# Performance work log

Measured on AMD Instinct MI355X. Metric: run time of the kernel, lower is better.

## Reference

```python
import jax, jax.numpy as jnp
import numpy as np

INF = 1e38  # matches torch source constant


def setup_inputs() -> dict:
    key = jax.random.key(0)
    k1, k2, k3 = jax.random.split(key, 3)
    B, N, D = 16, 2048, 512
    query = jax.random.normal(k1, (B, N, D), dtype=jnp.float32)
    # nn.Linear(dims, dims, bias=False): weight [out, in] = [D, D]
    W_in = jax.random.normal(k2, (D, D), dtype=jnp.float32) * (1.0 / np.sqrt(D))
    # nn.Linear(2*dims, dims, bias=False): weight [D, 2D]
    W_out = jax.random.normal(k3, (D, 2 * D), dtype=jnp.float32) * (1.0 / np.sqrt(2 * D))
    return {"query": query, "W_in": W_in, "W_out": W_out}


def reference(query, W_in, W_out):
    B, N, D = query.shape
    # linear_in: y = x @ W^T
    q = jnp.einsum("bnd,ed->bne", query, W_in)  # [B, N, D]
    # full QK^T scores
    scores = jnp.einsum("bnd,bmd->bnm", q, q)  # [B, N, N]
    # torch: scores[:, triu_mask] = -INF  -> mask upper triangle INCLUDING diagonal
    mask = jnp.triu(jnp.ones((N, N), dtype=bool))
    scores = jnp.where(mask, -INF, scores)
    weights = jax.nn.softmax(scores, axis=-1)
    # row 0 is all -INF -> softmax gives uniform; torch zeroes it explicitly
    weights = weights.at[:, 0, :].set(0.0)
    mix = jnp.einsum("bnm,bmd->bnd", weights, q)  # [B, N, D]
    combined = jnp.concatenate([mix, q], axis=-1)  # [B, N, 2D]
    # linear_out (no activation since activation=None)
    output = jnp.einsum("bnc,dc->bnd", combined, W_out)  # [B, N, D]
    return output
```

## Files before the change

kernel.cpp:

```cpp
#include <hip/hip_runtime.h>

typedef _Float16 f16;
typedef _Float16 half8 __attribute__((ext_vector_type(8)));
typedef _Float16 half4 __attribute__((ext_vector_type(4)));
typedef float floatx4 __attribute__((ext_vector_type(4)));
typedef unsigned int uintx4 __attribute__((ext_vector_type(4)));

#define MFMA16(a, b, c) __builtin_amdgcn_mfma_f32_16x16x32_f16(a, b, c, 0, 0, 0)

__device__ __forceinline__ void gload16(const void* g, void* l) {
    __builtin_amdgcn_global_load_lds((const __attribute__((address_space(1))) void*)g,
                                     (__attribute__((address_space(3))) void*)l, 16, 0, 0);
}

__global__ __launch_bounds__(256) void k_cvt(const float* __restrict__ query,
                                             const float* __restrict__ Wi,
                                             const float* __restrict__ Wo,
                                             f16* __restrict__ q16,
                                             f16* __restrict__ W16)
{
    int i = blockIdx.x * 256 + threadIdx.x;
    const float4* src;
    f16* dst;
    if (i < 4194304) { src = (const float4*)query + i; dst = q16 + (size_t)i * 4; }
    else if (i < 4259840) { int j = i - 4194304; src = (const float4*)Wi + j; dst = W16 + (size_t)j * 4; }
    else { int j = i - 4259840; src = (const float4*)Wo + j; dst = W16 + 262144 + (size_t)j * 4; }
    float4 v = *src;
    half4 h = {(f16)v.x, (f16)v.y, (f16)v.z, (f16)v.w};
    *reinterpret_cast<half4*>(dst) = h;
}

__global__ __launch_bounds__(256) void k_qin(const f16* __restrict__ q16,
                                             const f16* __restrict__ W16,
                                             f16* __restrict__ comb,
                                             f16* __restrict__ qT)
{
    __shared__ char sm[65536];
    const int tid = threadIdx.x, lane = tid & 63, w = tid >> 6;
    const int l15 = lane & 15, quad = lane >> 4;
    const int id = blockIdx.x, xcd = id & 7, u = id >> 3;
    const int mbase = (xcd * 32 + (u >> 2)) * 128;
    const int nbase = (u & 3) * 128;
    const int wm = (w & 1) * 64, wn = (w >> 1) * 64;
    const int ia = wm >> 4, jb = wn >> 4;

    floatx4 acc[4][4];
#pragma unroll
    for (int i = 0; i < 4; ++i)
#pragma unroll
        for (int j = 0; j < 4; ++j) acc[i][j] = (floatx4)0.f;

    auto STAGE = [&](int k0, int bsel) {
        f16* At = (f16*)(sm + bsel * 32768);
        f16* Bt = At + 8192;
#pragma unroll
        for (int jr = 0; jr < 4; ++jr) {
            int bi = jr * 4 + w, i2 = bi >> 1, s = bi & 1;
            gload16(q16 + (size_t)(mbase + i2 * 16 + l15) * 512 + k0 + s * 32 + quad * 8, At + bi * 512);
            gload16(W16 + (size_t)(nbase + i2 * 16 + l15) * 512 + k0 + s * 32 + quad * 8, Bt + bi * 512);
        }
    };

    STAGE(0, 0);
    __syncthreads();
    for (int it = 0; it < 8; ++it) {
        const int cur = it & 1;
        if (it < 7) STAGE((it + 1) * 64, cur ^ 1);
        f16* At = (f16*)(sm + cur * 32768);
        f16* Bt = At + 8192;
#pragma unroll
        for (int s = 0; s < 2; ++s) {
            half8 a[4], bf[4];
#pragma unroll
            for (int i = 0; i < 4; ++i)
                a[i] = *reinterpret_cast<half8*>(At + ((ia + i) * 2 + s) * 512 + lane * 8);
#pragma unroll
            for (int j = 0; j < 4; ++j)
                bf[j] = *reinterpret_cast<half8*>(Bt + ((jb + j) * 2 + s) * 512 + lane * 8);
#pragma unroll
            for (int i = 0; i < 4; ++i)
#pragma unroll
                for (int j = 0; j < 4; ++j)
                    acc[i][j] = MFMA16(a[i], bf[j], acc[i][j]);
        }
        __syncthreads();
    }
    const int bb = mbase >> 11, tb = mbase & 2047;
    f16* ct = (f16*)sm;
#pragma unroll
    for (int i = 0; i < 4; ++i)
#pragma unroll
        for (int j = 0; j < 4; ++j)
#pragma unroll
            for (int r = 0; r < 4; ++r)
                ct[(wm + i * 16 + quad * 4 + r) * 136 + wn + j * 16 + l15] = (f16)acc[i][j][r];
    __syncthreads();
#pragma unroll
    for (int it = 0; it < 8; ++it) {
        int c = it * 256 + tid, r = c >> 4, c8 = (c & 15) << 3;
        *reinterpret_cast<half8*>(comb + (size_t)(mbase + r) * 1024 + 512 + nbase + c8) =
            *reinterpret_cast<half8*>(ct + r * 136 + c8);
    }
    __syncthreads();
#pragma unroll
    for (int i = 0; i < 4; ++i)
#pragma unroll
        for (int j = 0; j < 4; ++j) {
            half4 h = {(f16)acc[i][j][0], (f16)acc[i][j][1], (f16)acc[i][j][2], (f16)acc[i][j][3]};
            *reinterpret_cast<half4*>(ct + (wn + j * 16 + l15) * 136 + wm + i * 16 + quad * 4) = h;
        }
    __syncthreads();
#pragma unroll
    for (int it = 0; it < 8; ++it) {
        int c = it * 256 + tid, dd = c >> 4, tc = (c & 15) << 3;
        *reinterpret_cast<half8*>(qT + ((size_t)bb * 512 + nbase + dd) * 2048 + tb + tc) =
            *reinterpret_cast<half8*>(ct + dd * 136 + tc);
    }
}

__global__ __launch_bounds__(256) void k_sgemmsm(const f16* __restrict__ comb,
                                                 f16* __restrict__ Pd,
                                                 float* __restrict__ Mt,
                                                 float* __restrict__ Lt)
{
    __shared__ char sm[65536];
    const int tid = threadIdx.x, lane = tid & 63, w = tid >> 6;
    const int l15 = lane & 15, quad = lane >> 4;
    const int wm = (w & 1) * 64, wn = (w >> 1) * 64;
    const int ia = wm >> 4, jb = wn >> 4;

    int bx = blockIdx.y, mt = 0;
    while ((mt + 1) * (mt + 2) / 2 <= bx) ++mt;
    const int nt = bx - mt * (mt + 1) / 2;
    const int b = blockIdx.x;
    const f16* qa = comb + ((size_t)b * 2048 + mt * 128) * 1024 + 512;
    const f16* qb = comb + ((size_t)b * 2048 + nt * 128) * 1024 + 512;

    floatx4 acc[4][4];
#pragma unroll
    for (int i = 0; i < 4; ++i)
#pragma unroll
        for (int j = 0; j < 4; ++j) acc[i][j] = (floatx4)0.f;

    auto STAGE = [&](int k0, int bsel) {
        f16* At = (f16*)(sm + bsel * 32768);
        f16* Bt = At + 8192;
#pragma unroll
        for (int jr = 0; jr < 4; ++jr) {
            int bi = jr * 4 + w, i2 = bi >> 1, s = bi & 1;
            gload16(qa + (size_t)(i2 * 16 + l15) * 1024 + k0 + s * 32 + quad * 8, At + bi * 512);
            gload16(qb + (size_t)(i2 * 16 + l15) * 1024 + k0 + s * 32 + quad * 8, Bt + bi * 512);
        }
    };

    STAGE(0, 0);
    __syncthreads();
    for (int it = 0; it < 8; ++it) {
        const int cur = it & 1;
        if (it < 7) STAGE((it + 1) * 64, cur ^ 1);
        f16* At = (f16*)(sm + cur * 32768);
        f16* Bt = At + 8192;
#pragma unroll
        for (int s = 0; s < 2; ++s) {
            half8 a[4], bf[4];
#pragma unroll
            for (int i = 0; i < 4; ++i)
                a[i] = *reinterpret_cast<half8*>(At + ((ia + i) * 2 + s) * 512 + lane * 8);
#pragma unroll
            for (int j = 0; j < 4; ++j)
                bf[j] = *reinterpret_cast<half8*>(Bt + ((jb + j) * 2 + s) * 512 + lane * 8);
#pragma unroll
            for (int i = 0; i < 4; ++i)
#pragma unroll
                for (int j = 0; j < 4; ++j)
                    acc[i][j] = MFMA16(a[i], bf[j], acc[i][j]);
        }
        __syncthreads();
    }

    const bool diag = (nt == mt);
    f16* ct = (f16*)sm;
    float* redm = (float*)(sm + 40960);
    float* reds = (float*)(sm + 43008);
    const int hb = w & 1;

    float wmax[4][4];
#pragma unroll
    for (int i = 0; i < 4; ++i)
#pragma unroll
        for (int r = 0; r < 4; ++r) {
            const int rowl = wm + i * 16 + quad * 4 + r;
            float mm = -1e38f;
#pragma unroll
            for (int j = 0; j < 4; ++j) {
                float v = acc[i][j][r];
                if (diag && (wn + j * 16 + l15) >= rowl) v = -1e38f;
                mm = fmaxf(mm, v);
            }
            mm = fmaxf(mm, __shfl_xor(mm, 1));
            mm = fmaxf(mm, __shfl_xor(mm, 2));
            mm = fmaxf(mm, __shfl_xor(mm, 4));
            mm = fmaxf(mm, __shfl_xor(mm, 8));
            wmax[i][r] = mm;
        }
    if (l15 == 0)
#pragma unroll
        for (int i = 0; i < 4; ++i)
#pragma unroll
            for (int r = 0; r < 4; ++r)
                redm[w * 64 + i * 16 + quad * 4 + r] = wmax[i][r];
    __syncthreads();

#pragma unroll
    for (int i = 0; i < 4; ++i)
#pragma unroll
        for (int r = 0; r < 4; ++r) {
            const int idx = i * 16 + quad * 4 + r;
            const int rowl = wm + idx;
            const float m = fmaxf(redm[hb * 64 + idx], redm[(hb + 2) * 64 + idx]);
            float ssum = 0.f;
#pragma unroll
            for (int j = 0; j < 4; ++j) {
                const int col = wn + j * 16 + l15;
                const bool valid = !diag || (col < rowl);
                float e = valid ? __expf(acc[i][j][r] - m) : 0.f;
                ssum += e;
                ct[rowl * 136 + col] = (f16)e;
            }
            ssum += __shfl_xor(ssum, 1);
            ssum += __shfl_xor(ssum, 2);
            ssum += __shfl_xor(ssum, 4);
            ssum += __shfl_xor(ssum, 8);
            wmax[i][r] = ssum;
        }
    if (l15 == 0)
#pragma unroll
        for (int i = 0; i < 4; ++i)
#pragma unroll
            for (int r = 0; r < 4; ++r)
                reds[w * 64 + i * 16 + quad * 4 + r] = wmax[i][r];
    __syncthreads();

    if (tid < 128) {
        const int h2 = tid >> 6, i2 = tid & 63;
        const float mm = fmaxf(redm[h2 * 64 + i2], redm[(h2 + 2) * 64 + i2]);
        const float ll = reds[h2 * 64 + i2] + reds[(h2 + 2) * 64 + i2];
        const size_t o = (((size_t)b * 16 + nt) << 11) + mt * 128 + tid;
        Mt[o] = mm;
        Lt[o] = ll;
    }
    f16* Pt = Pd + ((size_t)(b * 136 + bx) << 14);
#pragma unroll
    for (int itp = 0; itp < 8; ++itp) {
        int c = itp * 256 + tid, r_ = c >> 4, c8 = (c & 15) << 3;
        *reinterpret_cast<half8*>(Pt + r_ * 128 + c8) =
            *reinterpret_cast<half8*>(ct + r_ * 136 + c8);
    }
}

__global__ __launch_bounds__(256) void k_stats(float* Mt, const float* __restrict__ Lt)
{
    const int b = blockIdx.x, row = blockIdx.y * 256 + threadIdx.x;
    const int mtr = row >> 7;
    float mv[16], lv[16];
    for (int t = 0; t <= mtr; ++t) {
        const size_t o = (((size_t)b * 16 + t) << 11) + row;
        mv[t] = Mt[o];
        lv[t] = Lt[o];
    }
    float M = -1e38f;
    for (int t = 0; t <= mtr; ++t) M = fmaxf(M, mv[t]);
    float l = 0.f;
    for (int t = 0; t <= mtr; ++t) l += lv[t] * __expf(mv[t] - M);
    const float invl = (l > 0.f) ? 1.f / l : 0.f;
    for (int t = 0; t <= mtr; ++t)
        Mt[(((size_t)b * 16 + t) << 11) + row] = __expf(mv[t] - M) * invl;
}

__global__ __launch_bounds__(256) void k_pv(const f16* __restrict__ Pd,
                                            const f16* __restrict__ qT,
                                            f16* __restrict__ comb,
                                            const float* __restrict__ Ft)
{
    __shared__ char sm[65536];
    const int tid = threadIdx.x, lane = tid & 63, w = tid >> 6;
    const int l15 = lane & 15, quad = lane >> 4;
    const int wm = (w & 1) * 64, wn = (w >> 1) * 64;
    const int ia = wm >> 4, jb = wn >> 4;
    const int id = blockIdx.x;
    const int p = id & 7, nb = (id >> 3) & 3, b = id >> 5;
    const f16* Pdb = Pd + ((size_t)b * 136 << 14);
    const f16* qTb = qT + ((size_t)b * 512 + nb * 128) * 2048;

    for (int t = 0; t < 2; ++t) {
        const int mt = t ? (15 - p) : p;
        const int tb0 = mt * (mt + 1) / 2;
        const int kit = (mt + 1) * 2;

        floatx4 acc[4][4], accT[4][4];
#pragma unroll
        for (int i = 0; i < 4; ++i)
#pragma unroll
            for (int j = 0; j < 4; ++j) { acc[i][j] = (floatx4)0.f; accT[i][j] = (floatx4)0.f; }

        auto STAGE = [&](int it, int bsel) {
            f16* At = (f16*)(sm + bsel * 32768);
            f16* Bt = At + 8192;
            const int k0 = it * 64;
#pragma unroll
            for (int jr = 0; jr < 4; ++jr) {
                int bi = jr * 4 + w, i2 = bi >> 1, s = bi & 1;
                gload16(Pdb + ((size_t)(tb0 + (k0 >> 7)) << 14) + (size_t)(i2 * 16 + l15) * 128
                            + (k0 & 64) + s * 32 + quad * 8,
                        At + bi * 512);
                gload16(qTb + (size_t)(i2 * 16 + l15) * 2048 + k0 + s * 32 + quad * 8, Bt + bi * 512);
            }
        };

        STAGE(0, 0);
        __syncthreads();
        for (int it = 0; it < kit; ++it) {
            const int cur = it & 1;
            if (it + 1 < kit) STAGE(it + 1, cur ^ 1);
            f16* At = (f16*)(sm + cur * 32768);
            f16* Bt = At + 8192;
#pragma unroll
            for (int s = 0; s < 2; ++s) {
                half8 a[4], bf[4];
#pragma unroll
                for (int i = 0; i < 4; ++i)
                    a[i] = *reinterpret_cast<half8*>(At + ((ia + i) * 2 + s) * 512 + lane * 8);
#pragma unroll
                for (int j = 0; j < 4; ++j)
                    bf[j] = *reinterpret_cast<half8*>(Bt + ((jb + j) * 2 + s) * 512 + lane * 8);
#pragma unroll
                for (int i = 0; i < 4; ++i)
#pragma unroll
                    for (int j = 0; j < 4; ++j)
                        acc[i][j] = MFMA16(a[i], bf[j], acc[i][j]);
            }
            if (it & 1) {
                const int tt = it >> 1;
                const float* fp = Ft + (((size_t)b * 16 + tt) << 11) + mt * 128 + wm;
#pragma unroll
                for (int i = 0; i < 4; ++i) {
                    floatx4 fv = *reinterpret_cast<const floatx4*>(fp + i * 16 + quad * 4);
#pragma unroll
                    for (int j = 0; j < 4; ++j) {
                        accT[i][j] += acc[i][j] * fv;
                        acc[i][j] = (floatx4)0.f;
                    }
                }
            }
            __syncthreads();
        }

        f16* ct = (f16*)sm;
#pragma unroll
        for (int i = 0; i < 4; ++i)
#pragma unroll
            for (int j = 0; j < 4; ++j)
#pragma unroll
                for (int r = 0; r < 4; ++r)
                    ct[(wm + i * 16 + quad * 4 + r) * 136 + wn + j * 16 + l15] = (f16)accT[i][j][r];
        __syncthreads();
#pragma unroll
        for (int it = 0; it < 8; ++it) {
            int c = it * 256 + tid, r = c >> 4, c8 = (c & 15) << 3;
            *reinterpret_cast<half8*>(comb + ((size_t)b * 2048 + mt * 128 + r) * 1024 + nb * 128 + c8) =
                *reinterpret_cast<half8*>(ct + r * 136 + c8);
        }
        __syncthreads();
    }
}

__global__ __launch_bounds__(256) void k_out(const f16* __restrict__ comb,
                                             const f16* __restrict__ Wo16,
                                             float* __restrict__ out)
{
    __shared__ char sm[65536];
    const int tid = threadIdx.x, lane = tid & 63, w = tid >> 6;
    const int l15 = lane & 15, quad = lane >> 4;
    const int id = blockIdx.x, xcd = id & 7, u = id >> 3;
    const int mbase = (xcd * 32 + (u >> 2)) * 128;
    const int nbase = (u & 3) * 128;
    const int wm = (w & 1) * 64, wn = (w >> 1) * 64;
    const int ia = wm >> 4, jb = wn >> 4;

    floatx4 acc[4][4];
#pragma unroll
    for (int i = 0; i < 4; ++i)
#pragma unroll
        for (int j = 0; j < 4; ++j) acc[i][j] = (floatx4)0.f;

    auto STAGE = [&](int k0, int bsel) {
        f16* At = (f16*)(sm + bsel * 32768);
        f16* Bt = At + 8192;
#pragma unroll
        for (int jr = 0; jr < 4; ++jr) {
            int bi = jr * 4 + w, i2 = bi >> 1, s = bi & 1;
            gload16(comb + (size_t)(mbase + i2 * 16 + l15) * 1024 + k0 + s * 32 + quad * 8,
                    At + bi * 512);
            gload16(Wo16 + (size_t)(nbase + i2 * 16 + l15) * 1024 + k0 + s * 32 + quad * 8,
                    Bt + bi * 512);
        }
    };

    STAGE(0, 0);
    __syncthreads();
    for (int it = 0; it < 16; ++it) {
        const int cur = it & 1;
        if (it < 15) STAGE((it + 1) * 64, cur ^ 1);
        f16* At = (f16*)(sm + cur * 32768);
        f16* Bt = At + 8192;
#pragma unroll
        for (int s = 0; s < 2; ++s) {
            half8 a[4], bf[4];
#pragma unroll
            for (int i = 0; i < 4; ++i)
                a[i] = *reinterpret_cast<half8*>(At + ((ia + i) * 2 + s) * 512 + lane * 8);
#pragma unroll
            for (int j = 0; j < 4; ++j)
                bf[j] = *reinterpret_cast<half8*>(Bt + ((jb + j) * 2 + s) * 512 + lane * 8);
#pragma unroll
            for (int i = 0; i < 4; ++i)
#pragma unroll
                for (int j = 0; j < 4; ++j)
                    acc[i][j] = MFMA16(a[i], bf[j], acc[i][j]);
        }
        __syncthreads();
    }
    float* cf = (float*)sm;
    for (int pass = 0; pass < 2; ++pass) {
        __syncthreads();
        if ((w & 1) == pass) {
#pragma unroll
            for (int i = 0; i < 4; ++i)
#pragma unroll
                for (int j = 0; j < 4; ++j)
#pragma unroll
                    for (int r = 0; r < 4; ++r)
                        cf[(i * 16 + quad * 4 + r) * 132 + wn + j * 16 + l15] = acc[i][j][r];
        }
        __syncthreads();
#pragma unroll
        for (int it = 0; it < 8; ++it) {
            int c = it * 256 + tid, row = c >> 5, c4 = (c & 31) << 2;
            __builtin_nontemporal_store(
                *reinterpret_cast<floatx4*>(cf + row * 132 + c4),
                reinterpret_cast<floatx4*>(out + (size_t)(mbase + pass * 64 + row) * 512 + nbase + c4));
        }
    }
}

extern "C" void kernel_launch(void* const* d_in, const int* in_sizes, int n_in,
                              void* d_out, int out_size, void* d_ws, size_t ws_size,
                              hipStream_t stream)
{
    const float* query = (const float*)d_in[0];
    const float* W_in  = (const float*)d_in[1];
    const float* W_out = (const float*)d_in[2];
    float* out = (float*)d_out;

    const size_t XOFF = 102236160ull;
    f16* comb = (f16*)d_ws;
    f16* qT   = comb + (size_t)32768 * 1024;
    f16* W16  = qT + (size_t)16 * 512 * 2048;
    f16* q16  = (f16*)((char*)d_ws + XOFF);
    f16* Pd   = (f16*)((char*)d_ws + XOFF);
    float* Mt = (float*)((char*)d_ws + XOFF + 71303168ull);
    float* Lt = (float*)((char*)d_ws + XOFF + 73400320ull);

    k_cvt<<<17152, 256, 0, stream>>>(query, W_in, W_out, q16, W16);
    k_qin<<<1024, 256, 0, stream>>>(q16, W16, comb, qT);
    k_sgemmsm<<<dim3(16, 136), 256, 0, stream>>>(comb, Pd, Mt, Lt);
    k_stats<<<dim3(16, 8), 256, 0, stream>>>(Mt, Lt);
    k_pv<<<512, 256, 0, stream>>>(Pd, qT, comb, Mt);
    k_out<<<1024, 256, 0, stream>>>(comb, W16 + 262144, out);
}
```

Baseline: 429.4 us.

## Pipeline GEMM loads with vmcnt waits and prescale P tiles in separate kernel

All four MFMA GEMM loops now issue loads two stages ahead, replacing full __syncthreads with explicit vmcnt waits plus raw s_barrier so global-to-LDS loads overlap compute. The per-tile softmax rescale factor, previously applied to a second accumulator set inside k_pv, moves into a new k_pscale kernel that rescales the stored fp16 P tiles in place. This frees registers and work in the PV loop, at the cost of an extra read-modify-write pass over P and an extra rounding step on P.

Result: faster. 404.5 us (-5.8%).

```diff
diff --git a/kernel.cpp b/kernel.cpp
--- a/kernel.cpp
+++ b/kernel.cpp
@@ -4,9 +4,13 @@
 typedef _Float16 half8 __attribute__((ext_vector_type(8)));
 typedef _Float16 half4 __attribute__((ext_vector_type(4)));
 typedef float floatx4 __attribute__((ext_vector_type(4)));
-typedef unsigned int uintx4 __attribute__((ext_vector_type(4)));
 
 #define MFMA16(a, b, c) __builtin_amdgcn_mfma_f32_16x16x32_f16(a, b, c, 0, 0, 0)
+
+#define PHASE_WAIT_8()  do { asm volatile("s_waitcnt vmcnt(8)" ::: "memory"); \
+    __builtin_amdgcn_sched_barrier(0); __builtin_amdgcn_s_barrier(); } while (0)
+#define PHASE_WAIT_0()  do { asm volatile("s_waitcnt vmcnt(0)" ::: "memory"); \
+    __builtin_amdgcn_sched_barrier(0); __builtin_amdgcn_s_barrier(); } while (0)
 
 __device__ __forceinline__ void gload16(const void* g, void* l) {
     __builtin_amdgcn_global_load_lds((const __attribute__((address_space(1))) void*)g,
@@ -62,10 +66,10 @@
     };
 
     STAGE(0, 0);
-    __syncthreads();
+    STAGE(64, 1);
     for (int it = 0; it < 8; ++it) {
         const int cur = it & 1;
-        if (it < 7) STAGE((it + 1) * 64, cur ^ 1);
+        if (it < 7) PHASE_WAIT_8(); else PHASE_WAIT_0();
         f16* At = (f16*)(sm + cur * 32768);
         f16* Bt = At + 8192;
 #pragma unroll
@@ -83,7 +87,8 @@
                 for (int j = 0; j < 4; ++j)
                     acc[i][j] = MFMA16(a[i], bf[j], acc[i][j]);
         }
-        __syncthreads();
+        __builtin_amdgcn_s_barrier();
+        if (it + 2 < 8) STAGE((it + 2) * 64, cur);
     }
     const int bb = mbase >> 11, tb = mbase & 2047;
     f16* ct = (f16*)sm;
@@ -154,10 +159,10 @@
     };
 
     STAGE(0, 0);
-    __syncthreads();
+    STAGE(64, 1);
     for (int it = 0; it < 8; ++it) {
         const int cur = it & 1;
-        if (it < 7) STAGE((it + 1) * 64, cur ^ 1);
+        if (it < 7) PHASE_WAIT_8(); else PHASE_WAIT_0();
         f16* At = (f16*)(sm + cur * 32768);
         f16* Bt = At + 8192;
 #pragma unroll
@@ -175,7 +180,8 @@
                 for (int j = 0; j < 4; ++j)
                     acc[i][j] = MFMA16(a[i], bf[j], acc[i][j]);
         }
-        __syncthreads();
+        __builtin_amdgcn_s_barrier();
+        if (it + 2 < 8) STAGE((it + 2) * 64, cur);
     }
 
     const bool diag = (nt == mt);
@@ -277,10 +283,29 @@
         Mt[(((size_t)b * 16 + t) << 11) + row] = __expf(mv[t] - M) * invl;
 }
 
+__global__ __launch_bounds__(256) void k_pscale(f16* __restrict__ Pd,
+                                               const float* __restrict__ Ft)
+{
+    int bx = blockIdx.y, mt = 0;
+    while ((mt + 1) * (mt + 2) / 2 <= bx) ++mt;
+    const int nt = bx - mt * (mt + 1) / 2;
+    const int b = blockIdx.x;
+    const int tid = threadIdx.x;
+    const int row = tid >> 1, c0 = (tid & 1) * 64;
+    const float Fv = Ft[(((size_t)b * 16 + nt) << 11) + mt * 128 + row];
+    f16* Pt = Pd + ((size_t)(b * 136 + bx) << 14) + (size_t)row * 128 + c0;
+#pragma unroll
+    for (int c = 0; c < 8; ++c) {
+        half8 h = *reinterpret_cast<half8*>(Pt + c * 8);
+#pragma unroll
+        for (int e = 0; e < 8; ++e) h[e] = (f16)((float)h[e] * Fv);
+        *reinterpret_cast<half8*>(Pt + c * 8) = h;
+    }
+}
+
 __global__ __launch_bounds__(256) void k_pv(const f16* __restrict__ Pd,
                                             const f16* __restrict__ qT,
-                                            f16* __restrict__ comb,
-                                            const float* __restrict__ Ft)
+                                            f16* __restrict__ comb)
 {
     __shared__ char sm[65536];
     const int tid = threadIdx.x, lane = tid & 63, w = tid >> 6;
@@ -297,11 +322,11 @@
         const int tb0 = mt * (mt + 1) / 2;
         const int kit = (mt + 1) * 2;
 
-        floatx4 acc[4][4], accT[4][4];
+        floatx4 acc[4][4];
 #pragma unroll
         for (int i = 0; i < 4; ++i)
 #pragma unroll
-            for (int j = 0; j < 4; ++j) { acc[i][j] = (floatx4)0.f; accT[i][j] = (floatx4)0.f; }
+            for (int j = 0; j < 4; ++j) acc[i][j] = (floatx4)0.f;
 
         auto STAGE = [&](int it, int bsel) {
             f16* At = (f16*)(sm + bsel * 32768);
@@ -318,10 +343,10 @@
         };
 
         STAGE(0, 0);
-        __syncthreads();
+        STAGE(1, 1);
         for (int it = 0; it < kit; ++it) {
             const int cur = it & 1;
-            if (it + 1 < kit) STAGE(it + 1, cur ^ 1);
+            if (it < kit - 1) PHASE_WAIT_8(); else PHASE_WAIT_0();
             f16* At = (f16*)(sm + cur * 32768);
             f16* Bt = At + 8192;
 #pragma unroll
@@ -339,20 +364,8 @@
                     for (int j = 0; j < 4; ++j)
                         acc[i][j] = MFMA16(a[i], bf[j], acc[i][j]);
             }
-            if (it & 1) {
-                const int tt = it >> 1;
-                const float* fp = Ft + (((size_t)b * 16 + tt) << 11) + mt * 128 + wm;
-#pragma unroll
-                for (int i = 0; i < 4; ++i) {
-                    floatx4 fv = *reinterpret_cast<const floatx4*>(fp + i * 16 + quad * 4);
-#pragma unroll
-                    for (int j = 0; j < 4; ++j) {
-                        accT[i][j] += acc[i][j] * fv;
-                        acc[i][j] = (floatx4)0.f;
-                    }
-                }
-            }
-            __syncthreads();
+            __builtin_amdgcn_s_barrier();
+            if (it + 2 < kit) STAGE(it + 2, cur);
         }
 
         f16* ct = (f16*)sm;
@@ -362,7 +375,7 @@
             for (int j = 0; j < 4; ++j)
 #pragma unroll
                 for (int r = 0; r < 4; ++r)
-                    ct[(wm + i * 16 + quad * 4 + r) * 136 + wn + j * 16 + l15] = (f16)accT[i][j][r];
+                    ct[(wm + i * 16 + quad * 4 + r) * 136 + wn + j * 16 + l15] = (f16)acc[i][j][r];
         __syncthreads();
 #pragma unroll
         for (int it = 0; it < 8; ++it) {
@@ -407,10 +420,10 @@
     };
 
     STAGE(0, 0);
-    __syncthreads();
+    STAGE(64, 1);
     for (int it = 0; it < 16; ++it) {
         const int cur = it & 1;
-        if (it < 15) STAGE((it + 1) * 64, cur ^ 1);
+        if (it < 15) PHASE_WAIT_8(); else PHASE_WAIT_0();
         f16* At = (f16*)(sm + cur * 32768);
         f16* Bt = At + 8192;
 #pragma unroll
@@ -428,7 +441,8 @@
                 for (int j = 0; j < 4; ++j)
                     acc[i][j] = MFMA16(a[i], bf[j], acc[i][j]);
         }
-        __syncthreads();
+        __builtin_amdgcn_s_barrier();
+        if (it + 2 < 16) STAGE((it + 2) * 64, cur);
     }
     float* cf = (float*)sm;
     for (int pass = 0; pass < 2; ++pass) {
@@ -475,6 +489,7 @@
     k_qin<<<1024, 256, 0, stream>>>(q16, W16, comb, qT);
     k_sgemmsm<<<dim3(16, 136), 256, 0, stream>>>(comb, Pd, Mt, Lt);
     k_stats<<<dim3(16, 8), 256, 0, stream>>>(Mt, Lt);
-    k_pv<<<512, 256, 0, stream>>>(Pd, qT, comb, Mt);
+    k_pscale<<<dim3(16, 136), 256, 0, stream>>>(Pd, Mt);
+    k_pv<<<512, 256, 0, stream>>>(Pd, qT, comb);
     k_out<<<1024, 256, 0, stream>>>(comb, W16 + 262144, out);
 }
```
